# Kernel optimization log

Hardware: AMD Instinct MI355X
Metric: run time of the kernel (lower is better)

## Reference

```python
import jax, jax.numpy as jnp
import numpy as np

DIM, DEPTH, MULT = 512, 3, 4
E = 2 ** DEPTH            # 8 experts
HID = MULT * DIM          # 2048
B, S = 4, 1024


def setup_inputs() -> dict:
    key = jax.random.key(0)
    ks = jax.random.split(key, 7)
    sd = 1.0 / np.sqrt(DIM)
    sh = 1.0 / np.sqrt(HID)
    return {
        "x": jax.random.normal(ks[0], (B, S, DIM), dtype=jnp.float32),
        "rw": jax.random.normal(ks[1], (E - 1, DIM), dtype=jnp.float32) * sd,
        "rb": jax.random.normal(ks[2], (E - 1,), dtype=jnp.float32) * sd,
        "w1": jax.random.normal(ks[3], (E, DIM, HID), dtype=jnp.float32) * sd,
        "b1": jax.random.normal(ks[4], (E, HID), dtype=jnp.float32) * sd,
        "w2": jax.random.normal(ks[5], (E, HID, DIM), dtype=jnp.float32) * sh,
        "b2": jax.random.normal(ks[6], (E, DIM), dtype=jnp.float32) * sh,
    }


def _leaf_probs(flat_x, rw, rb):
    # Binary-tree soft routing: level d has 2**d routers at offset 2**d - 1.
    n_tok = flat_x.shape[0]
    leaf = jnp.ones((n_tok, 1), dtype=flat_x.dtype)
    for d in range(DEPTH):
        off, n = 2 ** d - 1, 2 ** d
        logits = flat_x @ rw[off:off + n].T + rb[off:off + n]   # [N, n]
        p = jax.nn.sigmoid(logits)
        # child probs: left = 1-p, right = p
        leaf = (leaf[:, :, None] * jnp.stack([1.0 - p, p], axis=2)).reshape(n_tok, 2 * n)
    return leaf  # [N, E]


def reference(x, rw, rb, w1, b1, w2, b2):
    b, s, dim = x.shape
    flat_x = x.reshape(b * s, dim)                               # [N, D]
    leaf_probs = _leaf_probs(flat_x, rw, rb)                     # [N, E]
    # Dense evaluation of all experts (soft-routing training path).
    h = jnp.einsum('nd,edh->neh', flat_x, w1) + b1[None]         # [N, E, H]
    h = jax.nn.gelu(h, approximate=False)                        # torch nn.GELU (erf)
    y = jnp.einsum('neh,ehd->ned', h, w2) + b2[None]             # [N, E, D]
    out = jnp.einsum('ned,ne->nd', y, leaf_probs)                # [N, D]
    return out.reshape(b, s, dim)
```

## Files before the change

### kernel.cpp

```cpp
#include <hip/hip_runtime.h>
#include <hip/hip_bf16.h>
#include <hip/hip_fp16.h>

#define DIM 512
#define HID 2048
#define NE 8
#define NTOK 4096

typedef _Float16 v8h __attribute__((ext_vector_type(8)));
typedef float v16f __attribute__((ext_vector_type(16)));

__device__ __forceinline__ void load16(const void* g, void* l) {
  __builtin_amdgcn_global_load_lds(
      (const __attribute__((address_space(1))) unsigned int*)g,
      (__attribute__((address_space(3))) unsigned int*)l, 16, 0, 0);
}

__device__ __forceinline__ float gelu_fast(float v) {
  float v2 = v * v;
  float u = v * __builtin_fmaf(0.07135481627f, v2, 1.5957691216f);
  float t = __expf(-u);
  return v * __builtin_amdgcn_rcpf(1.0f + t);
}

__global__ __launch_bounds__(256) void pre_kernel(const float* __restrict__ x,
                                                  const float* __restrict__ rw,
                                                  const float* __restrict__ rb,
                                                  const float* __restrict__ b2,
                                                  const float* __restrict__ w1,
                                                  const float* __restrict__ w2,
                                                  float* __restrict__ leaf,
                                                  _Float16* __restrict__ xh,
                                                  float* __restrict__ out,
                                                  _Float16* __restrict__ w1t,
                                                  _Float16* __restrict__ w2t) {
  __shared__ float tile[32][65];
  if (blockIdx.x < 1024) {
    const int lane = threadIdx.x & 63;
    const int wave = threadIdx.x >> 6;
    const int n = (blockIdx.x << 2) + wave;
    const float4* xv = (const float4*)(x + (size_t)n * DIM);
    const float4 x0 = xv[lane * 2], x1 = xv[lane * 2 + 1];
    v8h o;
    o[0] = (_Float16)x0.x; o[1] = (_Float16)x0.y; o[2] = (_Float16)x0.z; o[3] = (_Float16)x0.w;
    o[4] = (_Float16)x1.x; o[5] = (_Float16)x1.y; o[6] = (_Float16)x1.z; o[7] = (_Float16)x1.w;
    *(v8h*)(xh + (size_t)n * DIM + lane * 8) = o;
    float logits[7];
#pragma unroll
    for (int rr = 0; rr < 7; ++rr) {
      const float4* wv = (const float4*)(rw + rr * DIM);
      const float4 w0 = wv[lane * 2], w1v = wv[lane * 2 + 1];
      float s = x0.x * w0.x + x0.y * w0.y + x0.z * w0.z + x0.w * w0.w +
                x1.x * w1v.x + x1.y * w1v.y + x1.z * w1v.z + x1.w * w1v.w;
#pragma unroll
      for (int o2 = 32; o2; o2 >>= 1) s += __shfl_xor(s, o2, 64);
      logits[rr] = s + rb[rr];
    }
    const int eidx = lane & 7;
    const float p0 = 1.f / (1.f + __expf(-logits[0]));
    float f = ((eidx >> 2) & 1) ? p0 : 1.f - p0;
    const float p1 = 1.f / (1.f + __expf(-logits[1 + (eidx >> 2)]));
    f *= ((eidx >> 1) & 1) ? p1 : 1.f - p1;
    const float p2 = 1.f / (1.f + __expf(-logits[3 + (eidx >> 1)]));
    f *= (eidx & 1) ? p2 : 1.f - p2;
    if (lane < NE) leaf[(size_t)n * NE + lane] = f;
    float le[NE];
#pragma unroll
    for (int e = 0; e < NE; ++e) le[e] = __shfl(f, e, 64);
    float4 a0 = {0.f, 0.f, 0.f, 0.f}, a1 = {0.f, 0.f, 0.f, 0.f};
#pragma unroll
    for (int e = 0; e < NE; ++e) {
      const float4* bv = (const float4*)(b2 + (size_t)e * DIM + lane * 8);
      const float4 u0 = bv[0], u1 = bv[1];
      a0.x += le[e] * u0.x; a0.y += le[e] * u0.y; a0.z += le[e] * u0.z; a0.w += le[e] * u0.w;
      a1.x += le[e] * u1.x; a1.y += le[e] * u1.y; a1.z += le[e] * u1.z; a1.w += le[e] * u1.w;
    }
    float4* op = (float4*)(out + (size_t)n * DIM + lane * 8);
    op[0] = a0; op[1] = a1;
  } else {
    int bx = blockIdx.x - 1024;
    const float* in;
    _Float16* outp;
    int R, C;
    if (bx < 4096) { in = w1; outp = w1t; R = DIM; C = HID; }
    else { bx -= 4096; in = w2; outp = w2t; R = HID; C = DIM; }
    const int e = bx >> 9;
    const int rem = bx & 511;
    const int tiles_r = R >> 6;
    const int rt = rem % tiles_r;
    const int ct = rem / tiles_r;
    const int r0 = rt << 6, c0 = ct << 5;
    const size_t ebase = (size_t)e * R * C;
    const int tid = threadIdx.x;
#pragma unroll
    for (int it = 0; it < 2; ++it) {
      const int s = tid + (it << 8);
      const int row = s >> 3, cq = s & 7;
      const float4 v = *(const float4*)(in + ebase + (size_t)(r0 + row) * C + c0 + (cq << 2));
      tile[(cq << 2) + 0][row] = v.x;
      tile[(cq << 2) + 1][row] = v.y;
      tile[(cq << 2) + 2][row] = v.z;
      tile[(cq << 2) + 3][row] = v.w;
    }
    __syncthreads();
    const int c = tid >> 3, seg = tid & 7;
    v8h hv;
#pragma unroll
    for (int u = 0; u < 8; ++u) hv[u] = (_Float16)tile[c][(seg << 3) + u];
    *(v8h*)(outp + ebase + (size_t)(c0 + c) * R + r0 + (seg << 3)) = hv;
  }
}


#define GEMM_STAGE(AO_LDS, BO_LDS, KOFF)                                      \
  {                                                                           \
    _Pragma("unroll") for (int p = 0; p < 4; ++p)                             \
        load16(ga[p] + (KOFF), la[p] + (AO_LDS));                             \
    _Pragma("unroll") for (int p = 0; p < 2; ++p)                             \
        load16(gb[p] + (KOFF), lb[p] + (BO_LDS));                             \
  }

#define GEMM_COMPUTE(AO, BO)                                                  \
  {                                                                           \
    v8h a[4], b[2];                                                           \
    _Pragma("unroll") for (int i = 0; i < 4; ++i)                             \
        a[i] = *(const v8h*)(fA[i] + (AO) + po0);                             \
    _Pragma("unroll") for (int j = 0; j < 2; ++j)                             \
        b[j] = *(const v8h*)(fB[j] + (BO) + po0);                             \
    _Pragma("unroll") for (int i = 0; i < 4; ++i)                             \
        _Pragma("unroll") for (int j = 0; j < 2; ++j)                         \
            acc[i][j] = __builtin_amdgcn_mfma_f32_32x32x16_f16(a[i], b[j], acc[i][j], 0, 0, 0); \
    _Pragma("unroll") for (int i = 0; i < 4; ++i)                             \
        a[i] = *(const v8h*)(fA[i] + (AO) + (po0 ^ 16));                      \
    _Pragma("unroll") for (int j = 0; j < 2; ++j)                             \
        b[j] = *(const v8h*)(fB[j] + (BO) + (po0 ^ 16));                      \
    _Pragma("unroll") for (int i = 0; i < 4; ++i)                             \
        _Pragma("unroll") for (int j = 0; j < 2; ++j)                         \
            acc[i][j] = __builtin_amdgcn_mfma_f32_32x32x16_f16(a[i], b[j], acc[i][j], 0, 0, 0); \
  }

__global__ __launch_bounds__(256, 2) void gemm1_kernel(const _Float16* __restrict__ xh,
                                                       const _Float16* __restrict__ w1t,
                                                       const float* __restrict__ b1,
                                                       const float* __restrict__ leaf,
                                                       _Float16* __restrict__ H) {
  const int bx = blockIdx.x;
  const int e = bx & 7;
  const int t = bx >> 3;
  const int mt = t & 15;
  const int nt = t >> 4;
  const int m0 = mt << 8, n0 = nt << 7;

  __shared__ alignas(16) _Float16 As[2 * 256 * 32];
  __shared__ alignas(16) _Float16 Bs[2 * 128 * 32];

  const int tid = threadIdx.x;
  const int lane = tid & 63;
  const int wave = tid >> 6;
  const int wm = wave >> 1, wn = wave & 1;
  const int c = lane & 31, h2 = lane >> 5;
  const int swz = (c >> 1) & 3;
  const int po0 = (h2 ^ swz) << 3;

  const _Float16* ga[4];
  const _Float16* gb[2];
  _Float16* la[4];
  _Float16* lb[2];
#pragma unroll
  for (int p = 0; p < 4; ++p) {
    const int ci = (p << 8) + tid;
    const int row = ci >> 2;
    const int lg = (ci & 3) ^ ((row >> 1) & 3);
    ga[p] = xh + (size_t)(m0 + row) * DIM + (lg << 3);
    la[p] = As + (ci << 3);
  }
#pragma unroll
  for (int p = 0; p < 2; ++p) {
    const int ci = (p << 8) + tid;
    const int row = ci >> 2;
    const int lg = (ci & 3) ^ ((row >> 1) & 3);
    gb[p] = w1t + ((size_t)e * HID + n0 + row) * DIM + (lg << 3);
    lb[p] = Bs + (ci << 3);
  }
  const _Float16* fA[4];
  const _Float16* fB[2];
#pragma unroll
  for (int i = 0; i < 4; ++i) fA[i] = As + (((wm << 7) + (i << 5) + c) << 5);
#pragma unroll
  for (int j = 0; j < 2; ++j) fB[j] = Bs + (((wn << 6) + (j << 5) + c) << 5);

  v16f acc[4][2];
#pragma unroll
  for (int i = 0; i < 4; ++i)
#pragma unroll
    for (int j = 0; j < 2; ++j)
      acc[i][j] = v16f{0.f,0.f,0.f,0.f,0.f,0.f,0.f,0.f,0.f,0.f,0.f,0.f,0.f,0.f,0.f,0.f};

  GEMM_STAGE(0, 0, 0);
  __syncthreads();
  for (int gp = 0; gp < 7; ++gp) {
    GEMM_STAGE(8192, 4096, 32);
    GEMM_COMPUTE(0, 0);
    __syncthreads();
    GEMM_STAGE(0, 0, 64);
    GEMM_COMPUTE(8192, 4096);
    __syncthreads();
#pragma unroll
    for (int p = 0; p < 4; ++p) ga[p] += 64;
#pragma unroll
    for (int p = 0; p < 2; ++p) gb[p] += 64;
  }
  GEMM_STAGE(8192, 4096, 32);
  GEMM_COMPUTE(0, 0);
  __syncthreads();
  GEMM_COMPUTE(8192, 4096);

  const float* b1e = b1 + (size_t)e * HID;
  _Float16* He = H + (size_t)e * NTOK * HID;
  const int colb = n0 + (wn << 6) + c;
  const float bias0 = b1e[colb];
  const float bias1 = b1e[colb + 32];
#pragma unroll
  for (int i = 0; i < 4; ++i) {
    const int rb0 = m0 + (wm << 7) + (i << 5) + (h2 << 2);
#pragma unroll
    for (int rg = 0; rg < 4; ++rg) {
#pragma unroll
      for (int rr = 0; rr < 4; ++rr) {
        const int row = rb0 + (rg << 3) + rr;
        const int reg = (rg << 2) + rr;
        const float p = leaf[(size_t)row * NE + e];
        _Float16* hp = He + (size_t)row * HID + colb;
        hp[0]  = (_Float16)(p * gelu_fast(acc[i][0][reg] + bias0));
        hp[32] = (_Float16)(p * gelu_fast(acc[i][1][reg] + bias1));
      }
    }
  }
}

__global__ __launch_bounds__(256, 2) void gemm2_kernel(const _Float16* __restrict__ H,
                                                       const _Float16* __restrict__ w2t,
                                                       float* __restrict__ out) {
  const int bx = blockIdx.x;
  const int e = bx & 7;
  const int dt = (bx >> 3) & 3;
  const int mt = bx >> 5;
  const int m0 = mt << 8, d0 = dt << 7;

  __shared__ alignas(16) _Float16 As[2 * 256 * 32];
  __shared__ alignas(16) _Float16 Bs[2 * 128 * 32];

  const int tid = threadIdx.x;
  const int lane = tid & 63;
  const int wave = tid >> 6;
  const int wm = wave >> 1, wn = wave & 1;
  const int c = lane & 31, h2 = lane >> 5;
  const int swz = (c >> 1) & 3;
  const int po0 = (h2 ^ swz) << 3;

  const _Float16* ga[4];
  const _Float16* gb[2];
  _Float16* la[4];
  _Float16* lb[2];
#pragma unroll
  for (int p = 0; p < 4; ++p) {
    const int ci = (p << 8) + tid;
    const int row = ci >> 2;
    const int lg = (ci & 3) ^ ((row >> 1) & 3);
    ga[p] = H + ((size_t)e * NTOK + m0 + row) * HID + (lg << 3);
    la[p] = As + (ci << 3);
  }
#pragma unroll
  for (int p = 0; p < 2; ++p) {
    const int ci = (p << 8) + tid;
    const int row = ci >> 2;
    const int lg = (ci & 3) ^ ((row >> 1) & 3);
    gb[p] = w2t + ((size_t)e * DIM + d0 + row) * HID + (lg << 3);
    lb[p] = Bs + (ci << 3);
  }
  const _Float16* fA[4];
  const _Float16* fB[2];
#pragma unroll
  for (int i = 0; i < 4; ++i) fA[i] = As + (((wm << 7) + (i << 5) + c) << 5);
#pragma unroll
  for (int j = 0; j < 2; ++j) fB[j] = Bs + (((wn << 6) + (j << 5) + c) << 5);

  v16f acc[4][2];
#pragma unroll
  for (int i = 0; i < 4; ++i)
#pragma unroll
    for (int j = 0; j < 2; ++j)
      acc[i][j] = v16f{0.f,0.f,0.f,0.f,0.f,0.f,0.f,0.f,0.f,0.f,0.f,0.f,0.f,0.f,0.f,0.f};

  GEMM_STAGE(0, 0, 0);
  __syncthreads();
  for (int gp = 0; gp < 31; ++gp) {
    GEMM_STAGE(8192, 4096, 32);
    GEMM_COMPUTE(0, 0);
    __syncthreads();
    GEMM_STAGE(0, 0, 64);
    GEMM_COMPUTE(8192, 4096);
    __syncthreads();
#pragma unroll
    for (int p = 0; p < 4; ++p) ga[p] += 64;
#pragma unroll
    for (int p = 0; p < 2; ++p) gb[p] += 64;
  }
  GEMM_STAGE(8192, 4096, 32);
  GEMM_COMPUTE(0, 0);
  __syncthreads();
  GEMM_COMPUTE(8192, 4096);

#pragma unroll
  for (int i = 0; i < 4; ++i) {
    const int rb0 = m0 + (wm << 7) + (i << 5) + (h2 << 2);
#pragma unroll
    for (int rg = 0; rg < 4; ++rg) {
#pragma unroll
      for (int rr = 0; rr < 4; ++rr) {
        const int row = rb0 + (rg << 3) + rr;
        const int reg = (rg << 2) + rr;
        float* op = out + (size_t)row * DIM + d0 + (wn << 6) + c;
        atomicAdd(op, acc[i][0][reg]);
        atomicAdd(op + 32, acc[i][1][reg]);
      }
    }
  }
}

extern "C" void kernel_launch(void* const* d_in, const int* in_sizes, int n_in,
                              void* d_out, int out_size, void* d_ws, size_t ws_size,
                              hipStream_t stream) {
  const float* x  = (const float*)d_in[0];
  const float* rw = (const float*)d_in[1];
  const float* rb = (const float*)d_in[2];
  const float* w1 = (const float*)d_in[3];
  const float* b1 = (const float*)d_in[4];
  const float* w2 = (const float*)d_in[5];
  const float* b2 = (const float*)d_in[6];
  float* out = (float*)d_out;

  char* ws = (char*)d_ws;
  const size_t xh_bytes   = (size_t)NTOK * DIM * 2;
  const size_t w1t_bytes  = (size_t)NE * HID * DIM * 2;
  const size_t w2t_bytes  = (size_t)NE * DIM * HID * 2;
  const size_t leaf_bytes = (size_t)NTOK * NE * 4;
  const size_t H_bytes    = (size_t)NE * NTOK * HID * 2;
  _Float16* xh   = (_Float16*)(ws);
  _Float16* w1t  = (_Float16*)(ws + xh_bytes);
  _Float16* w2t  = (_Float16*)(ws + xh_bytes + w1t_bytes);
  float*    leaf = (float*)(ws + xh_bytes + w1t_bytes + w2t_bytes);
  _Float16* Hbuf = (_Float16*)(ws + xh_bytes + w1t_bytes + w2t_bytes + leaf_bytes);
  if (ws_size < xh_bytes + w1t_bytes + w2t_bytes + leaf_bytes + H_bytes) return;

  pre_kernel<<<9216, 256, 0, stream>>>(x, rw, rb, b2, w1, w2, leaf, xh, out, w1t, w2t);
  gemm1_kernel<<<2048, 256, 0, stream>>>(xh, w1t, b1, leaf, Hbuf);
  gemm2_kernel<<<512, 256, 0, stream>>>(Hbuf, w2t, out);
}
```

Before: 347.4 us.

## Deepen GEMM prefetch pipeline with manual vmcnt waits and MFMA priority

Restructures the double-buffered K-loop in both expert GEMM kernels so two stages of global-to-LDS loads are in flight, using explicit s_waitcnt vmcnt(6) and raw s_barrier instead of __syncthreads, which drains all outstanding loads. It also raises wave priority around the MFMA bursts with s_setprio. The goal is to hide global load latency behind matrix math. The cost is reliance on hand-counted outstanding loads (six per stage) for correctness, which could race if the compiler reorders or splits those loads.

```diff
diff --git a/kernel.cpp b/kernel.cpp
--- a/kernel.cpp
+++ b/kernel.cpp
@@ -112,6 +112,14 @@
 }
 
 
+#define WAITV6() asm volatile("s_waitcnt vmcnt(6)" ::: "memory")
+#define WAITV0() asm volatile("s_waitcnt vmcnt(0)" ::: "memory")
+#define BARF()                                                                \
+  {                                                                           \
+    __builtin_amdgcn_s_barrier();                                             \
+    asm volatile("" ::: "memory");                                            \
+  }
+
 #define GEMM_STAGE(AO_LDS, BO_LDS, KOFF)                                      \
   {                                                                           \
     _Pragma("unroll") for (int p = 0; p < 4; ++p)                             \
@@ -127,16 +135,42 @@
         a[i] = *(const v8h*)(fA[i] + (AO) + po0);                             \
     _Pragma("unroll") for (int j = 0; j < 2; ++j)                             \
         b[j] = *(const v8h*)(fB[j] + (BO) + po0);                             \
+    __builtin_amdgcn_s_setprio(1);                                            \
     _Pragma("unroll") for (int i = 0; i < 4; ++i)                             \
         _Pragma("unroll") for (int j = 0; j < 2; ++j)                         \
             acc[i][j] = __builtin_amdgcn_mfma_f32_32x32x16_f16(a[i], b[j], acc[i][j], 0, 0, 0); \
+    __builtin_amdgcn_s_setprio(0);                                            \
     _Pragma("unroll") for (int i = 0; i < 4; ++i)                             \
         a[i] = *(const v8h*)(fA[i] + (AO) + (po0 ^ 16));                      \
     _Pragma("unroll") for (int j = 0; j < 2; ++j)                             \
         b[j] = *(const v8h*)(fB[j] + (BO) + (po0 ^ 16));                      \
+    __builtin_amdgcn_s_setprio(1);                                            \
     _Pragma("unroll") for (int i = 0; i < 4; ++i)                             \
         _Pragma("unroll") for (int j = 0; j < 2; ++j)                         \
             acc[i][j] = __builtin_amdgcn_mfma_f32_32x32x16_f16(a[i], b[j], acc[i][j], 0, 0, 0); \
+    __builtin_amdgcn_s_setprio(0);                                            \
+  }
+
+#define GEMM_PIPE_ITER()                                                      \
+  {                                                                           \
+    WAITV6(); BARF();                                                         \
+    GEMM_COMPUTE(0, 0);                                                       \
+    BARF();                                                                   \
+    GEMM_STAGE(0, 0, 64);                                                     \
+    WAITV6(); BARF();                                                         \
+    GEMM_COMPUTE(8192, 4096);                                                 \
+    BARF();                                                                   \
+    GEMM_STAGE(8192, 4096, 96);                                               \
+    _Pragma("unroll") for (int p = 0; p < 4; ++p) ga[p] += 64;                \
+    _Pragma("unroll") for (int p = 0; p < 2; ++p) gb[p] += 64;                \
+  }
+
+#define GEMM_PIPE_TAIL()                                                      \
+  {                                                                           \
+    WAITV6(); BARF();                                                         \
+    GEMM_COMPUTE(0, 0);                                                       \
+    WAITV0(); BARF();                                                         \
+    GEMM_COMPUTE(8192, 4096);                                                 \
   }
 
 __global__ __launch_bounds__(256, 2) void gemm1_kernel(const _Float16* __restrict__ xh,
@@ -197,23 +231,9 @@
       acc[i][j] = v16f{0.f,0.f,0.f,0.f,0.f,0.f,0.f,0.f,0.f,0.f,0.f,0.f,0.f,0.f,0.f,0.f};
 
   GEMM_STAGE(0, 0, 0);
-  __syncthreads();
-  for (int gp = 0; gp < 7; ++gp) {
-    GEMM_STAGE(8192, 4096, 32);
-    GEMM_COMPUTE(0, 0);
-    __syncthreads();
-    GEMM_STAGE(0, 0, 64);
-    GEMM_COMPUTE(8192, 4096);
-    __syncthreads();
-#pragma unroll
-    for (int p = 0; p < 4; ++p) ga[p] += 64;
-#pragma unroll
-    for (int p = 0; p < 2; ++p) gb[p] += 64;
-  }
   GEMM_STAGE(8192, 4096, 32);
-  GEMM_COMPUTE(0, 0);
-  __syncthreads();
-  GEMM_COMPUTE(8192, 4096);
+  for (int gp = 0; gp < 7; ++gp) GEMM_PIPE_ITER();
+  GEMM_PIPE_TAIL();
 
   const float* b1e = b1 + (size_t)e * HID;
   _Float16* He = H + (size_t)e * NTOK * HID;
@@ -293,23 +313,9 @@
       acc[i][j] = v16f{0.f,0.f,0.f,0.f,0.f,0.f,0.f,0.f,0.f,0.f,0.f,0.f,0.f,0.f,0.f,0.f};
 
   GEMM_STAGE(0, 0, 0);
-  __syncthreads();
-  for (int gp = 0; gp < 31; ++gp) {
-    GEMM_STAGE(8192, 4096, 32);
-    GEMM_COMPUTE(0, 0);
-    __syncthreads();
-    GEMM_STAGE(0, 0, 64);
-    GEMM_COMPUTE(8192, 4096);
-    __syncthreads();
-#pragma unroll
-    for (int p = 0; p < 4; ++p) ga[p] += 64;
-#pragma unroll
-    for (int p = 0; p < 2; ++p) gb[p] += 64;
-  }
   GEMM_STAGE(8192, 4096, 32);
-  GEMM_COMPUTE(0, 0);
-  __syncthreads();
-  GEMM_COMPUTE(8192, 4096);
+  for (int gp = 0; gp < 31; ++gp) GEMM_PIPE_ITER();
+  GEMM_PIPE_TAIL();
 
 #pragma unroll
   for (int i = 0; i < 4; ++i) {
```

After: 350.4 us. No clear change (+0.9%).
